# Optimization experiments

Hardware: AMD Instinct MI355X
Metric: run time of the kernel (lower is better)

## Reference

```python
import jax, jax.numpy as jnp
import numpy as np

N = 500_000      # nodes
E = 8_000_000    # edges
F1 = 5           # num_features
F2 = 10          # num_features * 2
G = 8192         # number of graphs
GD = 10          # global_dim
BN_EPS = 1e-5


def _lin(key, fin, fout):
    kw, kb = jax.random.split(key)
    s = 1.0 / np.sqrt(fin)
    w = jax.random.uniform(kw, (fin, fout), jnp.float32, -s, s)
    b = jax.random.uniform(kb, (fout,), jnp.float32, -s, s)
    return w, b


def setup_inputs() -> dict:
    key = jax.random.key(0)
    ks = jax.random.split(key, 16)
    x = jax.random.normal(ks[0], (N, F1), jnp.float32)
    edge_index = jax.random.randint(ks[1], (2, E), 0, N, jnp.int32)
    batch = jnp.sort(jax.random.randint(ks[2], (N,), 0, G, jnp.int32))
    global_x = jax.random.normal(ks[3], (G, GD), jnp.float32)
    w11, b11 = _lin(ks[4], F1, F1)
    w12, b12 = _lin(ks[5], F1, F1)
    w21, b21 = _lin(ks[6], F1, F2)
    w22, b22 = _lin(ks[7], F2, F2)
    w31, b31 = _lin(ks[8], F2, F2)
    w32, b32 = _lin(ks[9], F2, F2)
    g1, be1 = jnp.ones((F1,), jnp.float32), jnp.zeros((F1,), jnp.float32)
    g2, be2 = jnp.ones((F2,), jnp.float32), jnp.zeros((F2,), jnp.float32)
    g3, be3 = jnp.ones((F2,), jnp.float32), jnp.zeros((F2,), jnp.float32)
    fw1, fb1 = _lin(ks[10], F2 + GD, 128)
    fw2, fb2 = _lin(ks[11], 128, 64)
    fw3, fb3 = _lin(ks[12], 64, 1)
    return dict(x=x, edge_index=edge_index, batch=batch, global_x=global_x,
                w11=w11, b11=b11, w12=w12, b12=b12,
                w21=w21, b21=b21, w22=w22, b22=b22,
                w31=w31, b31=b31, w32=w32, b32=b32,
                g1=g1, be1=be1, g2=g2, be2=be2, g3=g3, be3=be3,
                fw1=fw1, fb1=fb1, fw2=fw2, fb2=fb2, fw3=fw3, fb3=fb3)


def _gin(x, src, dst, w1, b1, w2, b2):
    # GINConv, eps=0: h = mlp(x + sum_{j->i} x_j)
    agg = jax.ops.segment_sum(x[src], dst, num_segments=N)
    h = x + agg
    h = jax.nn.relu(h @ w1 + b1)
    return h @ w2 + b2


def _bn(x, gamma, beta):
    # BatchNorm1d, training-mode batch statistics (biased var)
    mu = jnp.mean(x, axis=0)
    var = jnp.mean(jnp.square(x - mu), axis=0)
    return (x - mu) * jax.lax.rsqrt(var + BN_EPS) * gamma + beta


def reference(x, edge_index, batch, global_x,
              w11, b11, w12, b12, w21, b21, w22, b22, w31, b31, w32, b32,
              g1, be1, g2, be2, g3, be3,
              fw1, fb1, fw2, fb2, fw3, fb3):
    src, dst = edge_index[0], edge_index[1]
    h = _bn(jax.nn.relu(_gin(x, src, dst, w11, b11, w12, b12)), g1, be1)
    h = _bn(jax.nn.relu(_gin(h, src, dst, w21, b21, w22, b22)), g2, be2)
    h = _bn(jax.nn.relu(_gin(h, src, dst, w31, b31, w32, b32)), g3, be3)
    # global average pool over graphs
    sums = jax.ops.segment_sum(h, batch, num_segments=G)
    cnt = jax.ops.segment_sum(jnp.ones((h.shape[0],), h.dtype), batch, num_segments=G)
    pooled = sums / jnp.maximum(cnt, 1.0)[:, None]
    # dropout -> identity (eval)
    z = jnp.concatenate([pooled, global_x], axis=1)
    z = jax.nn.relu(z @ fw1 + fb1)
    z = jax.nn.relu(z @ fw2 + fb2)
    return z @ fw3 + fb3
```

## Files before the change

kernel.cpp:

```cpp
#include <hip/hip_runtime.h>


#define TF1 5
#define TF2 10
#define TGD 10
#define BN_EPS 1e-5f

typedef unsigned char u8;
typedef unsigned short u16;
typedef unsigned int u32;

__device__ __forceinline__ float bf2f(u32 u) {
  union { float f; u32 v; } c; c.v = u << 16; return c.f;
}
__device__ __forceinline__ u16 f2bf(float f) {
  union { float f; u32 v; } c; c.f = f;
  u32 u = c.v;
  u += 0x7fffu + ((u >> 16) & 1u);
  return (u16)(u >> 16);
}

template<int FIN, int FINS>
__device__ __forceinline__ void load_row(const float* __restrict__ h, long idx,
                                         float (&v)[FIN]) {
  const float* p = h + idx * FINS;
  if constexpr (FIN == 5 && FINS == 8) {
    float4 a = *(const float4*)p;
    v[0] = a.x; v[1] = a.y; v[2] = a.z; v[3] = a.w; v[4] = p[4];
  } else if constexpr (FIN == 10 && FINS == 10) {
    #pragma unroll
    for (int k = 0; k < 5; ++k) {
      float2 a = *(const float2*)(p + 2 * k);
      v[2 * k] = a.x; v[2 * k + 1] = a.y;
    }
  } else {
    #pragma unroll
    for (int f = 0; f < FIN; ++f) v[f] = p[f];
  }
}

template<int F, int BROW>
__device__ __forceinline__ void load_bf16_row(const u16* __restrict__ hb,
                                              long idx, float (&v)[F]) {
  if constexpr (BROW == 8) {
    uint4 w = *(const uint4*)(hb + idx * 8);
    v[0] = bf2f(w.x & 0xffffu); v[1] = bf2f(w.x >> 16);
    v[2] = bf2f(w.y & 0xffffu); v[3] = bf2f(w.y >> 16);
    v[4] = bf2f(w.z & 0xffffu);
  } else {
    uint4 wa = *(const uint4*)(hb + idx * 16);
    uint2 wb = *(const uint2*)(hb + idx * 16 + 8);
    v[0] = bf2f(wa.x & 0xffffu); v[1] = bf2f(wa.x >> 16);
    v[2] = bf2f(wa.y & 0xffffu); v[3] = bf2f(wa.y >> 16);
    v[4] = bf2f(wa.z & 0xffffu); v[5] = bf2f(wa.z >> 16);
    v[6] = bf2f(wa.w & 0xffffu); v[7] = bf2f(wa.w >> 16);
    v[8] = bf2f(wb.x & 0xffffu); v[9] = bf2f(wb.x >> 16);
  }
}

template<int F, int BROW>
__device__ __forceinline__ void store_bf16_row(u16* __restrict__ hb, long idx,
                                               const float* r) {
  if constexpr (BROW == 8) {
    uint4 w;
    w.x = (u32)f2bf(r[0]) | ((u32)f2bf(r[1]) << 16);
    w.y = (u32)f2bf(r[2]) | ((u32)f2bf(r[3]) << 16);
    w.z = (u32)f2bf(r[4]);
    w.w = 0u;
    *(uint4*)(hb + idx * 8) = w;
  } else {
    uint4 w;
    w.x = (u32)f2bf(r[0]) | ((u32)f2bf(r[1]) << 16);
    w.y = (u32)f2bf(r[2]) | ((u32)f2bf(r[3]) << 16);
    w.z = (u32)f2bf(r[4]) | ((u32)f2bf(r[5]) << 16);
    w.w = (u32)f2bf(r[6]) | ((u32)f2bf(r[7]) << 16);
    *(uint4*)(hb + idx * 16) = w;
    u32 w2 = (u32)f2bf(r[8]) | ((u32)f2bf(r[9]) << 16);
    *(u32*)(hb + idx * 16 + 8) = w2;
  }
}

__global__ __launch_bounds__(256) void prep_x_k(const float* __restrict__ x,
                                                u16* __restrict__ xb, int Nn) {
  int i = blockIdx.x * 256 + threadIdx.x;
  if (i >= Nn) return;
  float r[5];
  #pragma unroll
  for (int f = 0; f < 5; ++f) r[f] = x[(long)i * 5 + f];
  store_bf16_row<5, 8>(xb, i, r);
}

__global__ __launch_bounds__(256) void rank_k(const int* __restrict__ ei,
                                              int* __restrict__ deg,
                                              u8* __restrict__ rank, int E) {
  int e = blockIdx.x * blockDim.x + threadIdx.x;
  if (e >= E) return;
  rank[e] = (u8)atomicAdd(&deg[ei[E + e]], 1);
}

__global__ __launch_bounds__(256) void scan1_k(const int* __restrict__ deg,
                                               int* __restrict__ exc,
                                               int* __restrict__ bsum, int n) {
  __shared__ int lds[256];
  int t = threadIdx.x;
  int base = blockIdx.x * 2048 + t * 8;
  int v[8]; int local = 0;
  #pragma unroll
  for (int k = 0; k < 8; ++k) {
    int idx = base + k;
    v[k] = (idx < n) ? deg[idx] : 0;
    local += v[k];
  }
  lds[t] = local;
  __syncthreads();
  for (int off = 1; off < 256; off <<= 1) {
    int x = (t >= off) ? lds[t - off] : 0;
    __syncthreads();
    lds[t] += x;
    __syncthreads();
  }
  int running = lds[t] - local;
  #pragma unroll
  for (int k = 0; k < 8; ++k) {
    int idx = base + k;
    if (idx < n) exc[idx] = running;
    running += v[k];
  }
  if (t == 255) bsum[blockIdx.x] = lds[255];
}

__global__ __launch_bounds__(256) void scan2_k(int* __restrict__ bsum, int nb) {
  __shared__ int lds[256];
  int t = threadIdx.x;
  int v = (t < nb) ? bsum[t] : 0;
  lds[t] = v;
  __syncthreads();
  for (int off = 1; off < 256; off <<= 1) {
    int x = (t >= off) ? lds[t - off] : 0;
    __syncthreads();
    lds[t] += x;
    __syncthreads();
  }
  if (t < nb) bsum[t] = lds[t] - v;
}

__global__ __launch_bounds__(256) void scan3_k(int* __restrict__ exc,
                                               const int* __restrict__ bsum,
                                               int n) {
  int i = blockIdx.x * blockDim.x + threadIdx.x;
  if (i < n) exc[i] += bsum[i >> 11];
}

__global__ __launch_bounds__(256) void place2_k(const int* __restrict__ ei,
                                                const int* __restrict__ start,
                                                const u8* __restrict__ rank,
                                                int* __restrict__ colidx, int E) {
  int e = blockIdx.x * blockDim.x + threadIdx.x;
  if (e >= E) return;
  int s = ei[e];
  int d = ei[E + e];
  colidx[start[d] + (int)rank[e]] = s;
}

template<int FIN, int FINS, int BROW, int FHID, int FOUT, int FOUTS, int BROWOUT, bool BN>
__global__ __launch_bounds__(256) void gin2_k(
    const float* __restrict__ hf, const u16* __restrict__ hb,
    const int* __restrict__ deg, const int* __restrict__ rowstart,
    const int* __restrict__ colidx, const float* __restrict__ ssin,
    const float* __restrict__ w1, const float* __restrict__ b1,
    const float* __restrict__ w2, const float* __restrict__ b2,
    float* __restrict__ houtf, u16* __restrict__ houtb,
    float* __restrict__ part, int nblk, int Nn) {
  __shared__ float sw1[FIN * FHID], sb1[FHID], sw2[FHID * FOUT], sb2[FOUT];
  __shared__ float sred[4][FOUT], sredq[4][FOUT];
  int t = threadIdx.x;
  for (int i = t; i < FIN * FHID; i += 256) sw1[i] = w1[i];
  for (int i = t; i < FHID * FOUT; i += 256) sw2[i] = w2[i];
  if (t < FHID) sb1[t] = b1[t];
  if (t < FOUT) sb2[t] = b2[t];
  __syncthreads();

  float psum[FOUT], psq[FOUT];
  #pragma unroll
  for (int j = 0; j < FOUT; ++j) { psum[j] = 0.f; psq[j] = 0.f; }

  int i = blockIdx.x * 256 + t;
  if (i < Nn) {
    float acc[FIN];
    #pragma unroll
    for (int f = 0; f < FIN; ++f) acc[f] = 0.f;
    int st = rowstart[i];
    int d = deg[i];
    for (int p = st; p < st + d; ++p) {
      int s = colidx[p];
      float tv[FIN];
      load_bf16_row<FIN, BROW>(hb, s, tv);
      #pragma unroll
      for (int f = 0; f < FIN; ++f) acc[f] += tv[f];
    }
    float self[FIN];
    load_row<FIN, FINS>(hf, i, self);
    float xin[FIN];
    #pragma unroll
    for (int f = 0; f < FIN; ++f) {
      float a = acc[f] + self[f];
      if (BN) xin[f] = a * ssin[f] + (float)(d + 1) * ssin[FIN + f];
      else    xin[f] = a;
    }
    float u[FHID];
    #pragma unroll
    for (int j = 0; j < FHID; ++j) {
      float a = sb1[j];
      #pragma unroll
      for (int f = 0; f < FIN; ++f) a += xin[f] * sw1[f * FHID + j];
      u[j] = fmaxf(a, 0.f);
    }
    float rr[FOUT];
    #pragma unroll
    for (int j = 0; j < FOUT; ++j) {
      float a = sb2[j];
      #pragma unroll
      for (int k = 0; k < FHID; ++k) a += u[k] * sw2[k * FOUT + j];
      float r = fmaxf(a, 0.f);
      rr[j] = r;
      houtf[(long)i * FOUTS + j] = r;
      psum[j] = r;
      psq[j] = r * r;
    }
    if constexpr (BROWOUT > 0) store_bf16_row<FOUT, BROWOUT>(houtb, i, rr);
  }

  int lane = t & 63;
  int w = t >> 6;
  #pragma unroll
  for (int j = 0; j < FOUT; ++j) {
    float a = psum[j], b = psq[j];
    #pragma unroll
    for (int o = 32; o > 0; o >>= 1) {
      a += __shfl_down(a, o);
      b += __shfl_down(b, o);
    }
    if (lane == 0) { sred[w][j] = a; sredq[w][j] = b; }
  }
  __syncthreads();
  if (t < FOUT) {
    float s = sred[0][t] + sred[1][t] + sred[2][t] + sred[3][t];
    float q = sredq[0][t] + sredq[1][t] + sredq[2][t] + sredq[3][t];
    part[(size_t)t * nblk + blockIdx.x] = s;
    part[(size_t)(FOUT + t) * nblk + blockIdx.x] = q;
  }
}

__global__ __launch_bounds__(256) void bn_fin2_k(
    const float* __restrict__ part, int nblk,
    const float* __restrict__ gamma, const float* __restrict__ beta,
    float* __restrict__ ss, int F, double invN) {
  __shared__ double sfin[2 * TF2];
  __shared__ double wred[4];
  int t = threadIdx.x;
  for (int j = 0; j < 2 * F; ++j) {
    double s = 0.0;
    for (int b = t; b < nblk; b += 256) s += (double)part[(size_t)j * nblk + b];
    #pragma unroll
    for (int o = 32; o > 0; o >>= 1) s += __shfl_down(s, o);
    if ((t & 63) == 0) wred[t >> 6] = s;
    __syncthreads();
    if (t == 0) sfin[j] = wred[0] + wred[1] + wred[2] + wred[3];
    __syncthreads();
  }
  if (t < F) {
    float mu = (float)(sfin[t] * invN);
    float ex2 = (float)(sfin[F + t] * invN);
    float var = ex2 - mu * mu;
    float rstd = rsqrtf(var + BN_EPS);
    float sc = rstd * gamma[t];
    ss[t] = sc;
    ss[F + t] = beta[t] - mu * sc;
  }
}

template<int F, bool BN>
__global__ __launch_bounds__(256) void edge_agg_k(
    const int* __restrict__ ei, const float* __restrict__ h,
    const float* __restrict__ ss, float* __restrict__ agg, int E) {
  int e = blockIdx.x * blockDim.x + threadIdx.x;
  if (e >= E) return;
  int s = ei[e];
  int d = ei[E + e];
  #pragma unroll
  for (int f = 0; f < F; ++f) {
    float v = h[(long)s * F + f];
    if (BN) v = v * ss[f] + ss[F + f];
    atomicAdd(&agg[(long)d * F + f], v);
  }
}

template<int FIN, int FHID, int FOUT, bool BN>
__global__ __launch_bounds__(256) void gin_s_k(
    const float* __restrict__ h, const float* __restrict__ agg,
    const float* __restrict__ ssin,
    const float* __restrict__ w1, const float* __restrict__ b1,
    const float* __restrict__ w2, const float* __restrict__ b2,
    float* __restrict__ hout, float* __restrict__ part, int nblk, int Nn) {
  __shared__ float sw1[FIN * FHID], sb1[FHID], sw2[FHID * FOUT], sb2[FOUT];
  __shared__ float sred[4][FOUT], sredq[4][FOUT];
  int t = threadIdx.x;
  for (int i = t; i < FIN * FHID; i += 256) sw1[i] = w1[i];
  for (int i = t; i < FHID * FOUT; i += 256) sw2[i] = w2[i];
  if (t < FHID) sb1[t] = b1[t];
  if (t < FOUT) sb2[t] = b2[t];
  __syncthreads();

  float psum[FOUT], psq[FOUT];
  #pragma unroll
  for (int j = 0; j < FOUT; ++j) { psum[j] = 0.f; psq[j] = 0.f; }

  int i = blockIdx.x * 256 + t;
  if (i < Nn) {
    float xin[FIN];
    #pragma unroll
    for (int f = 0; f < FIN; ++f) {
      float v = h[(long)i * FIN + f];
      if (BN) v = v * ssin[f] + ssin[FIN + f];
      xin[f] = v + agg[(long)i * FIN + f];
    }
    float u[FHID];
    #pragma unroll
    for (int j = 0; j < FHID; ++j) {
      float a = sb1[j];
      #pragma unroll
      for (int f = 0; f < FIN; ++f) a += xin[f] * sw1[f * FHID + j];
      u[j] = fmaxf(a, 0.f);
    }
    #pragma unroll
    for (int j = 0; j < FOUT; ++j) {
      float a = sb2[j];
      #pragma unroll
      for (int k = 0; k < FHID; ++k) a += u[k] * sw2[k * FOUT + j];
      float r = fmaxf(a, 0.f);
      hout[(long)i * FOUT + j] = r;
      psum[j] = r;
      psq[j] = r * r;
    }
  }

  int lane = t & 63;
  int w = t >> 6;
  #pragma unroll
  for (int j = 0; j < FOUT; ++j) {
    float a = psum[j], b = psq[j];
    #pragma unroll
    for (int o = 32; o > 0; o >>= 1) {
      a += __shfl_down(a, o);
      b += __shfl_down(b, o);
    }
    if (lane == 0) { sred[w][j] = a; sredq[w][j] = b; }
  }
  __syncthreads();
  if (t < FOUT) {
    float s = sred[0][t] + sred[1][t] + sred[2][t] + sred[3][t];
    float q = sredq[0][t] + sredq[1][t] + sredq[2][t] + sredq[3][t];
    part[(size_t)t * nblk + blockIdx.x] = s;
    part[(size_t)(FOUT + t) * nblk + blockIdx.x] = q;
  }
}

__global__ __launch_bounds__(256) void pool_k(
    const float* __restrict__ h, const float* __restrict__ ss,
    const int* __restrict__ batch, float* __restrict__ z, int Nn, int Gn) {
  int g = blockIdx.x * 4 + (threadIdx.x >> 6);
  if (g >= Gn) return;
  int lane = threadIdx.x & 63;
  int lo = 0, hi = Nn;
  while (lo < hi) { int m = (lo + hi) >> 1; if (batch[m] < g) lo = m + 1; else hi = m; }
  int start = lo;
  hi = Nn;
  while (lo < hi) { int m = (lo + hi) >> 1; if (batch[m] < g + 1) lo = m + 1; else hi = m; }
  int end = lo;

  float acc[TF2];
  #pragma unroll
  for (int f = 0; f < TF2; ++f) acc[f] = 0.f;
  for (int i = start + lane; i < end; i += 64) {
    #pragma unroll
    for (int f = 0; f < TF2; ++f) acc[f] += h[(long)i * TF2 + f];
  }
  #pragma unroll
  for (int f = 0; f < TF2; ++f) {
    #pragma unroll
    for (int o = 32; o > 0; o >>= 1) acc[f] += __shfl_down(acc[f], o);
  }
  if (lane == 0) {
    int cnt = end - start;
    float inv = cnt > 0 ? 1.f / (float)cnt : 0.f;
    #pragma unroll
    for (int f = 0; f < TF2; ++f) {
      float m = acc[f] * inv;
      z[(long)g * TF2 + f] = cnt > 0 ? m * ss[f] + ss[TF2 + f] : 0.f;
    }
  }
}

__global__ __launch_bounds__(128) void final_mlp_k(
    const float* __restrict__ z10, const float* __restrict__ gx,
    const float* __restrict__ fw1, const float* __restrict__ fb1,
    const float* __restrict__ fw2, const float* __restrict__ fb2,
    const float* __restrict__ fw3, const float* __restrict__ fb3,
    float* __restrict__ out) {
  int g = blockIdx.x;
  int t = threadIdx.x;
  __shared__ float z[TF2 + TGD];
  __shared__ float h1[128];
  __shared__ float h2[64];
  if (t < TF2) z[t] = z10[(long)g * TF2 + t];
  else if (t < TF2 + TGD) z[t] = gx[(long)g * TGD + (t - TF2)];
  __syncthreads();
  {
    float a = fb1[t];
    #pragma unroll
    for (int i = 0; i < TF2 + TGD; ++i) a += z[i] * fw1[i * 128 + t];
    h1[t] = fmaxf(a, 0.f);
  }
  __syncthreads();
  if (t < 64) {
    float a = fb2[t];
    #pragma unroll 8
    for (int i = 0; i < 128; ++i) a += h1[i] * fw2[i * 64 + t];
    h2[t] = fmaxf(a, 0.f);
  }
  __syncthreads();
  if (t == 0) {
    float a = fb3[0];
    #pragma unroll 8
    for (int i = 0; i < 64; ++i) a += h2[i] * fw3[i];
    out[g] = a;
  }
}

extern "C" void kernel_launch(void* const* d_in, const int* in_sizes, int n_in,
                              void* d_out, int out_size, void* d_ws, size_t ws_size,
                              hipStream_t stream) {
  const float* x      = (const float*)d_in[0];
  const int*   ei     = (const int*)d_in[1];
  const int*   batch  = (const int*)d_in[2];
  const float* gx     = (const float*)d_in[3];
  const float* w11 = (const float*)d_in[4],  *b11 = (const float*)d_in[5];
  const float* w12 = (const float*)d_in[6],  *b12 = (const float*)d_in[7];
  const float* w21 = (const float*)d_in[8],  *b21 = (const float*)d_in[9];
  const float* w22 = (const float*)d_in[10], *b22 = (const float*)d_in[11];
  const float* w31 = (const float*)d_in[12], *b31 = (const float*)d_in[13];
  const float* w32 = (const float*)d_in[14], *b32 = (const float*)d_in[15];
  const float* g1  = (const float*)d_in[16], *be1 = (const float*)d_in[17];
  const float* g2  = (const float*)d_in[18], *be2 = (const float*)d_in[19];
  const float* g3  = (const float*)d_in[20], *be3 = (const float*)d_in[21];
  const float* fw1 = (const float*)d_in[22], *fb1 = (const float*)d_in[23];
  const float* fw2 = (const float*)d_in[24], *fb2 = (const float*)d_in[25];
  const float* fw3 = (const float*)d_in[26], *fb3 = (const float*)d_in[27];

  const int N = in_sizes[0] / TF1;
  const int E = in_sizes[1] / 2;
  const int G = in_sizes[3] / TGD;

  float* out = (float*)d_out;
  const int TB = 256;
  const int egrid = (E + TB - 1) / TB;
  const int ngrid = (N + TB - 1) / TB;
  const int pgrid = (G + 3) / 4;
  const double invN = 1.0 / (double)N;

  size_t sz_bufA = (size_t)N * 10 * sizeof(float);
  size_t sz_h2f  = (size_t)N * 10 * sizeof(float);
  size_t sz_xb   = (size_t)N * 8 * sizeof(u16);
  size_t sz_h1b  = (size_t)N * 8 * sizeof(u16);
  size_t sz_h2b  = (size_t)N * 16 * sizeof(u16);
  size_t sz_col  = (size_t)E * 4;
  size_t sz_deg  = (size_t)N * 4;
  size_t sz_cur  = (size_t)N * 4;
  size_t sz_rank = (size_t)E;
  size_t sz_bsum = 4096;
  size_t sz_part = (size_t)2 * TF2 * ngrid * sizeof(float);
  size_t small   = 3 * 2 * TF2 * sizeof(float) + (size_t)G * TF2 * sizeof(float) + 1024;
  size_t need_new = sz_bufA + sz_h2f + sz_xb + sz_h1b + sz_h2b + sz_col
                  + sz_deg + sz_cur + sz_rank + sz_bsum + sz_part + small;

  if (ws_size >= need_new) {
    char* ws = (char*)d_ws;
    float* bufA = (float*)ws;  ws += sz_bufA;
    float* h2f  = (float*)ws;  ws += sz_h2f;
    u16* xb     = (u16*)ws;    ws += sz_xb;
    u16* h1b    = (u16*)ws;    ws += sz_h1b;
    u16* h2b    = (u16*)ws;    ws += sz_h2b;
    int* colidx = (int*)ws;    ws += sz_col;
    int* deg    = (int*)ws;    ws += sz_deg;
    int* rowst  = (int*)ws;    ws += sz_cur;
    int* bsum   = (int*)ws;    ws += sz_bsum;
    float* part = (float*)ws;  ws += sz_part;
    float* ss1  = (float*)ws;  ws += 2 * TF2 * sizeof(float);
    float* ss2  = (float*)ws;  ws += 2 * TF2 * sizeof(float);
    float* ss3  = (float*)ws;  ws += 2 * TF2 * sizeof(float);
    float* z    = (float*)ws;  ws += (size_t)G * TF2 * sizeof(float);
    u8* rank    = (u8*)ws;     ws += sz_rank;

    hipMemsetAsync(deg, 0, sz_deg, stream);

    prep_x_k<<<ngrid, TB, 0, stream>>>(x, xb, N);

    rank_k<<<egrid, TB, 0, stream>>>(ei, deg, rank, E);
    int nb = (N + 2047) / 2048;
    scan1_k<<<nb, TB, 0, stream>>>(deg, rowst, bsum, N);
    scan2_k<<<1, TB, 0, stream>>>(bsum, nb);
    scan3_k<<<ngrid, TB, 0, stream>>>(rowst, bsum, N);
    place2_k<<<egrid, TB, 0, stream>>>(ei, rowst, rank, colidx, E);

    gin2_k<TF1, TF1, 8, TF1, TF1, 8, 8, false><<<ngrid, TB, 0, stream>>>(
        x, xb, deg, rowst, colidx, nullptr, w11, b11, w12, b12,
        bufA, h1b, part, ngrid, N);
    bn_fin2_k<<<1, TB, 0, stream>>>(part, ngrid, g1, be1, ss1, TF1, invN);

    gin2_k<TF1, 8, 8, TF2, TF2, TF2, 16, true><<<ngrid, TB, 0, stream>>>(
        bufA, h1b, deg, rowst, colidx, ss1, w21, b21, w22, b22,
        h2f, h2b, part, ngrid, N);
    bn_fin2_k<<<1, TB, 0, stream>>>(part, ngrid, g2, be2, ss2, TF2, invN);

    gin2_k<TF2, TF2, 16, TF2, TF2, TF2, 0, true><<<ngrid, TB, 0, stream>>>(
        h2f, h2b, deg, rowst, colidx, ss2, w31, b31, w32, b32,
        bufA, (u16*)nullptr, part, ngrid, N);
    bn_fin2_k<<<1, TB, 0, stream>>>(part, ngrid, g3, be3, ss3, TF2, invN);

    pool_k<<<pgrid, TB, 0, stream>>>(bufA, ss3, batch, z, N, G);
    final_mlp_k<<<G, 128, 0, stream>>>(z, gx, fw1, fb1, fw2, fb2, fw3, fb3, out);
  } else {
    char* ws = (char*)d_ws;
    float* agg = (float*)ws;  ws += (size_t)N * TF2 * sizeof(float);
    float* hA  = (float*)ws;  ws += (size_t)N * TF2 * sizeof(float);
    float* hB  = (float*)ws;  ws += (size_t)N * TF2 * sizeof(float);
    float* part = (float*)ws; ws += (size_t)2 * TF2 * ngrid * sizeof(float);
    float* ss1 = (float*)ws;   ws += 2 * TF2 * sizeof(float);
    float* ss2 = (float*)ws;   ws += 2 * TF2 * sizeof(float);
    float* ss3 = (float*)ws;   ws += 2 * TF2 * sizeof(float);
    float* z   = (float*)ws;

    hipMemsetAsync(agg, 0, (size_t)N * TF1 * sizeof(float), stream);
    edge_agg_k<TF1, false><<<egrid, TB, 0, stream>>>(ei, x, nullptr, agg, E);
    gin_s_k<TF1, TF1, TF1, false><<<ngrid, TB, 0, stream>>>(
        x, agg, nullptr, w11, b11, w12, b12, hA, part, ngrid, N);
    bn_fin2_k<<<1, TB, 0, stream>>>(part, ngrid, g1, be1, ss1, TF1, invN);

    hipMemsetAsync(agg, 0, (size_t)N * TF1 * sizeof(float), stream);
    edge_agg_k<TF1, true><<<egrid, TB, 0, stream>>>(ei, hA, ss1, agg, E);
    gin_s_k<TF1, TF2, TF2, true><<<ngrid, TB, 0, stream>>>(
        hA, agg, ss1, w21, b21, w22, b22, hB, part, ngrid, N);
    bn_fin2_k<<<1, TB, 0, stream>>>(part, ngrid, g2, be2, ss2, TF2, invN);

    hipMemsetAsync(agg, 0, (size_t)N * TF2 * sizeof(float), stream);
    edge_agg_k<TF2, true><<<egrid, TB, 0, stream>>>(ei, hB, ss2, agg, E);
    gin_s_k<TF2, TF2, TF2, true><<<ngrid, TB, 0, stream>>>(
        hB, agg, ss2, w31, b31, w32, b32, hA, part, ngrid, N);
    bn_fin2_k<<<1, TB, 0, stream>>>(part, ngrid, g3, be3, ss3, TF2, invN);

    pool_k<<<pgrid, TB, 0, stream>>>(hA, ss3, batch, z, N, G);
    final_mlp_k<<<G, 128, 0, stream>>>(z, gx, fw1, fb1, fw2, fb2, fw3, fb3, out);
  }
}
```

Baseline: 1.398 ms.

## Split each node's neighbor gather across four lanes with shuffle reduction

The GIN aggregation kernel now assigns four threads per node instead of one. The threads stride over the CSR neighbor list and combine their partial sums with xor shuffles, and lane 0 runs the MLP and the stores. The goal is more memory-level parallelism and less per-thread serial latency in the gather, which averages about 16 neighbors per node. The cost is four times as many blocks, a larger partial-stats buffer for batch norm, and three idle lanes during the MLP phase.

```diff
diff --git a/kernel.cpp b/kernel.cpp
--- a/kernel.cpp
+++ b/kernel.cpp
@@ -163,7 +163,7 @@
 }
 
 template<int FIN, int FINS, int BROW, int FHID, int FOUT, int FOUTS, int BROWOUT, bool BN>
-__global__ __launch_bounds__(256) void gin2_k(
+__global__ __launch_bounds__(256) void gin4_k(
     const float* __restrict__ hf, const u16* __restrict__ hb,
     const int* __restrict__ deg, const int* __restrict__ rowstart,
     const int* __restrict__ colidx, const float* __restrict__ ssin,
@@ -184,50 +184,59 @@
   #pragma unroll
   for (int j = 0; j < FOUT; ++j) { psum[j] = 0.f; psq[j] = 0.f; }
 
-  int i = blockIdx.x * 256 + t;
-  if (i < Nn) {
+  int node = blockIdx.x * 64 + (t >> 2);
+  int sub = t & 3;
+  if (node < Nn) {
     float acc[FIN];
     #pragma unroll
     for (int f = 0; f < FIN; ++f) acc[f] = 0.f;
-    int st = rowstart[i];
-    int d = deg[i];
-    for (int p = st; p < st + d; ++p) {
+    int st = rowstart[node];
+    int d = deg[node];
+    for (int p = st + sub; p < st + d; p += 4) {
       int s = colidx[p];
       float tv[FIN];
       load_bf16_row<FIN, BROW>(hb, s, tv);
       #pragma unroll
       for (int f = 0; f < FIN; ++f) acc[f] += tv[f];
     }
-    float self[FIN];
-    load_row<FIN, FINS>(hf, i, self);
-    float xin[FIN];
     #pragma unroll
     for (int f = 0; f < FIN; ++f) {
-      float a = acc[f] + self[f];
-      if (BN) xin[f] = a * ssin[f] + (float)(d + 1) * ssin[FIN + f];
-      else    xin[f] = a;
-    }
-    float u[FHID];
-    #pragma unroll
-    for (int j = 0; j < FHID; ++j) {
-      float a = sb1[j];
+      acc[f] += __shfl_xor(acc[f], 1);
+      acc[f] += __shfl_xor(acc[f], 2);
+    }
+
+    if (sub == 0) {
+      float self[FIN];
+      load_row<FIN, FINS>(hf, node, self);
+      float xin[FIN];
       #pragma unroll
-      for (int f = 0; f < FIN; ++f) a += xin[f] * sw1[f * FHID + j];
-      u[j] = fmaxf(a, 0.f);
-    }
-    float rr[FOUT];
-    #pragma unroll
-    for (int j = 0; j < FOUT; ++j) {
-      float a = sb2[j];
+      for (int f = 0; f < FIN; ++f) {
+        float a = acc[f] + self[f];
+        if (BN) xin[f] = a * ssin[f] + (float)(d + 1) * ssin[FIN + f];
+        else    xin[f] = a;
+      }
+      float u[FHID];
       #pragma unroll
-      for (int k = 0; k < FHID; ++k) a += u[k] * sw2[k * FOUT + j];
-      float r = fmaxf(a, 0.f);
-      rr[j] = r;
-      houtf[(long)i * FOUTS + j] = r;
-      psum[j] = r;
-      psq[j] = r * r;
-    }
-    if constexpr (BROWOUT > 0) store_bf16_row<FOUT, BROWOUT>(houtb, i, rr);
+      for (int j = 0; j < FHID; ++j) {
+        float a = sb1[j];
+        #pragma unroll
+        for (int f = 0; f < FIN; ++f) a += xin[f] * sw1[f * FHID + j];
+        u[j] = fmaxf(a, 0.f);
+      }
+      float rr[FOUT];
+      #pragma unroll
+      for (int j = 0; j < FOUT; ++j) {
+        float a = sb2[j];
+        #pragma unroll
+        for (int k = 0; k < FHID; ++k) a += u[k] * sw2[k * FOUT + j];
+        float r = fmaxf(a, 0.f);
+        rr[j] = r;
+        houtf[(long)node * FOUTS + j] = r;
+        psum[j] = r;
+        psq[j] = r * r;
+      }
+      if constexpr (BROWOUT > 0) store_bf16_row<FOUT, BROWOUT>(houtb, node, rr);
+    }
   }
 
   int lane = t & 63;
@@ -465,6 +474,7 @@
   const int TB = 256;
   const int egrid = (E + TB - 1) / TB;
   const int ngrid = (N + TB - 1) / TB;
+  const int g4grid = (N + 63) / 64;
   const int pgrid = (G + 3) / 4;
   const double invN = 1.0 / (double)N;
 
@@ -478,7 +488,7 @@
   size_t sz_cur  = (size_t)N * 4;
   size_t sz_rank = (size_t)E;
   size_t sz_bsum = 4096;
-  size_t sz_part = (size_t)2 * TF2 * ngrid * sizeof(float);
+  size_t sz_part = (size_t)2 * TF2 * g4grid * sizeof(float);
   size_t small   = 3 * 2 * TF2 * sizeof(float) + (size_t)G * TF2 * sizeof(float) + 1024;
   size_t need_new = sz_bufA + sz_h2f + sz_xb + sz_h1b + sz_h2b + sz_col
                   + sz_deg + sz_cur + sz_rank + sz_bsum + sz_part + small;
@@ -512,20 +522,20 @@
     scan3_k<<<ngrid, TB, 0, stream>>>(rowst, bsum, N);
     place2_k<<<egrid, TB, 0, stream>>>(ei, rowst, rank, colidx, E);
 
-    gin2_k<TF1, TF1, 8, TF1, TF1, 8, 8, false><<<ngrid, TB, 0, stream>>>(
+    gin4_k<TF1, TF1, 8, TF1, TF1, 8, 8, false><<<g4grid, TB, 0, stream>>>(
         x, xb, deg, rowst, colidx, nullptr, w11, b11, w12, b12,
-        bufA, h1b, part, ngrid, N);
-    bn_fin2_k<<<1, TB, 0, stream>>>(part, ngrid, g1, be1, ss1, TF1, invN);
-
-    gin2_k<TF1, 8, 8, TF2, TF2, TF2, 16, true><<<ngrid, TB, 0, stream>>>(
+        bufA, h1b, part, g4grid, N);
+    bn_fin2_k<<<1, TB, 0, stream>>>(part, g4grid, g1, be1, ss1, TF1, invN);
+
+    gin4_k<TF1, 8, 8, TF2, TF2, TF2, 16, true><<<g4grid, TB, 0, stream>>>(
         bufA, h1b, deg, rowst, colidx, ss1, w21, b21, w22, b22,
-        h2f, h2b, part, ngrid, N);
-    bn_fin2_k<<<1, TB, 0, stream>>>(part, ngrid, g2, be2, ss2, TF2, invN);
-
-    gin2_k<TF2, TF2, 16, TF2, TF2, TF2, 0, true><<<ngrid, TB, 0, stream>>>(
+        h2f, h2b, part, g4grid, N);
+    bn_fin2_k<<<1, TB, 0, stream>>>(part, g4grid, g2, be2, ss2, TF2, invN);
+
+    gin4_k<TF2, TF2, 16, TF2, TF2, TF2, 0, true><<<g4grid, TB, 0, stream>>>(
         h2f, h2b, deg, rowst, colidx, ss2, w31, b31, w32, b32,
-        bufA, (u16*)nullptr, part, ngrid, N);
-    bn_fin2_k<<<1, TB, 0, stream>>>(part, ngrid, g3, be3, ss3, TF2, invN);
+        bufA, (u16*)nullptr, part, g4grid, N);
+    bn_fin2_k<<<1, TB, 0, stream>>>(part, g4grid, g3, be3, ss3, TF2, invN);
 
     pool_k<<<pgrid, TB, 0, stream>>>(bufA, ss3, batch, z, N, G);
     final_mlp_k<<<G, 128, 0, stream>>>(z, gx, fw1, fb1, fw2, fb2, fw3, fb3, out);
```

After: 1.454 ms. 1.04x slower.
